# Optimization experiments

Measured on AMD Instinct MI355X. Metric: run time of the kernel, lower is better.

Reference implementation:

```python
import jax, jax.numpy as jnp
import numpy as np

NUM_EXPERTS = 8
HIDDEN = 2048
FFN = 1376
CAPACITY_FACTOR = 1.25
SCORE_SCALE = 1.0


def setup_inputs() -> dict:
    key = jax.random.key(0)
    k = jax.random.split(key, 6)
    T = 8192
    x = jax.random.normal(k[0], (T, HIDDEN), dtype=jnp.float32)
    topK_indices = jax.random.randint(k[1], (T,), 0, NUM_EXPERTS, dtype=jnp.int64)
    topK_scores = jax.random.uniform(k[2], (T,), dtype=jnp.float32)
    s = 1.0 / np.sqrt(HIDDEN)
    w_gate = jax.random.normal(k[3], (NUM_EXPERTS, HIDDEN, FFN), dtype=jnp.float32) * s
    w_up = jax.random.normal(k[4], (NUM_EXPERTS, HIDDEN, FFN), dtype=jnp.float32) * s
    w_down = jax.random.normal(k[5], (NUM_EXPERTS, FFN, HIDDEN), dtype=jnp.float32) * (1.0 / np.sqrt(FFN))
    return {"x": x, "topK_indices": topK_indices, "topK_scores": topK_scores,
            "w_gate": w_gate, "w_up": w_up, "w_down": w_down}


def reference(x, topK_indices, topK_scores, w_gate, w_up, w_down):
    T, D = x.shape
    E = w_gate.shape[0]
    capacity = int(CAPACITY_FACTOR * T / E)  # static (depends only on shapes)
    # position of each token within its assigned expert (deterministic drop:
    # keep the first `capacity` tokens in sequence order per expert)
    oh = jax.nn.one_hot(topK_indices, E, dtype=jnp.int32)          # [T,E]
    rank = jnp.take_along_axis(jnp.cumsum(oh, axis=0) - 1,
                               topK_indices[:, None].astype(jnp.int32), axis=1)[:, 0]
    keep = rank < capacity                                          # [T]
    # dispatch into per-expert capacity buffers; dropped tokens go to dummy slot
    slot = jnp.where(keep, topK_indices.astype(jnp.int32) * capacity + rank, E * capacity)
    buf = jnp.zeros((E * capacity + 1, D), x.dtype)
    buf = buf.at[slot].set(jnp.where(keep[:, None], x, jnp.zeros_like(x)))
    xe = buf[:E * capacity].reshape(E, capacity, D)                 # [E,C,D]
    # per-expert SwiGLU MLP as grouped GEMMs
    h = jax.nn.silu(jnp.einsum('ecd,edf->ecf', xe, w_gate)) * jnp.einsum('ecd,edf->ecf', xe, w_up)
    out = jnp.einsum('ecf,efd->ecd', h, w_down).reshape(E * capacity, D)
    out = jnp.concatenate([out, jnp.zeros((1, D), out.dtype)], axis=0)
    # combine: dropped tokens -> zero (dropped_padding='zero'), gate-score fusion
    y = out[slot] * keep[:, None].astype(out.dtype)
    y = y * (topK_scores[:, None] * SCORE_SCALE)
    return y
```

## Files before the change

### kernel.cpp

```cpp
#include <hip/hip_runtime.h>
#include <hip/hip_bf16.h>
#include <cstdint>
#include <cstddef>

#define NTOK 8192
#define DH   2048
#define DF   1376
#define NE   8
#define CAP  1280

typedef __bf16 bf16x8 __attribute__((ext_vector_type(8)));
typedef float  f32x4  __attribute__((ext_vector_type(4)));

#define BARRIER() asm volatile("s_barrier" ::: "memory")
#define WAITV(n)  asm volatile("s_waitcnt vmcnt(" #n ")" ::: "memory")
#define LGKM(n)   asm volatile("s_waitcnt lgkmcnt(" #n ")" ::: "memory")
#define SCHED0()  __builtin_amdgcn_sched_barrier(0)
#define SETPRIO(n) __builtin_amdgcn_s_setprio(n)

__device__ __forceinline__ uint32_t pk2(float a, float b) {
  float2 f; f.x = a; f.y = b;
  union { __hip_bfloat162 h; uint32_t u; } cv;
  cv.h = __float22bfloat162_rn(f);
  return cv.u;
}
__device__ __forceinline__ ushort bf16bits(float a) {
  return (ushort)(pk2(a, 0.f) & 0xFFFFu);
}
__device__ __forceinline__ void gload16(const ushort* g, ushort* l) {
  __builtin_amdgcn_global_load_lds(
      (const __attribute__((address_space(1))) uint32_t*)(const void*)g,
      (__attribute__((address_space(3))) uint32_t*)(void*)l,
      16, 0, 0);
}

__device__ __forceinline__ void rp_src(int o, int& row, int& ko) {
  int p = o >> 7;
  int g = ((o >> 4) & 7) ^ (p & 7);
  row = p * 2 + (g >> 2);
  ko  = (g & 3) * 8;
}
__device__ __forceinline__ int rp_off(int row, int l4) {
  return ((row >> 1) << 7) + (((((row & 1) << 2) + l4) ^ ((row >> 1) & 7)) << 4);
}

__global__ void routing_kernel(const int* __restrict__ idx, int* __restrict__ tok_slot,
                               int* __restrict__ tok_keep) {
  __shared__ int cnt[256][NE];
  const int t = threadIdx.x;
  for (int s = t; s < NE * CAP; s += 256) tok_slot[s] = -1;
  unsigned long long cA = 0ull, cB = 0ull;
  const int per = NTOK / 256, base = t * per;
  for (int i = 0; i < per; ++i) {
    int e = idx[base + i];
    unsigned long long inc = 1ull << ((e & 3) * 16);
    if (e < 4) cA += inc; else cB += inc;
  }
#pragma unroll
  for (int e = 0; e < 4; ++e) cnt[t][e]     = (int)((cA >> (e * 16)) & 0xFFFF);
#pragma unroll
  for (int e = 0; e < 4; ++e) cnt[t][4 + e] = (int)((cB >> (e * 16)) & 0xFFFF);
  __syncthreads();
  if (t < NE) {
    int run = 0;
    for (int i = 0; i < 256; ++i) { int c = cnt[i][t]; cnt[i][t] = run; run += c; }
  }
  __syncthreads();
  cA = 0ull; cB = 0ull;
#pragma unroll
  for (int e = 0; e < 4; ++e) cA |= (unsigned long long)(cnt[t][e] & 0xFFFF) << (e * 16);
#pragma unroll
  for (int e = 0; e < 4; ++e) cB |= (unsigned long long)(cnt[t][4 + e] & 0xFFFF) << (e * 16);
  for (int i = 0; i < per; ++i) {
    int token = base + i;
    int e = idx[token];
    int sh = (e & 3) * 16;
    int r = (int)(((e < 4 ? cA : cB) >> sh) & 0xFFFF);
    unsigned long long inc = 1ull << sh;
    if (e < 4) cA += inc; else cB += inc;
    bool keep = (r < CAP);
    tok_keep[token] = keep ? 1 : 0;
    if (keep) tok_slot[e * CAP + r] = token;
  }
}

__global__ __launch_bounds__(256) void prep_all(
    const float* __restrict__ wg, const float* __restrict__ wu, const float* __restrict__ wd,
    ushort* __restrict__ wgt, ushort* __restrict__ wut, ushort* __restrict__ wdt,
    const float* __restrict__ x, const int* __restrict__ keep,
    ushort* __restrict__ xb, float* __restrict__ y) {
  const int z = blockIdx.z;
  const int tid = threadIdx.x;
  if (z >= 24) {
    const int row = (z - 24) * 1024 + blockIdx.y * 32 + blockIdx.x;
    const int c = tid * 8;
    const size_t off = (size_t)row * DH + c;
    float4 a = *(const float4*)(x + off);
    float4 b = *(const float4*)(x + off + 4);
    uint4 p = { pk2(a.x, a.y), pk2(a.z, a.w), pk2(b.x, b.y), pk2(b.z, b.w) };
    *(uint4*)(xb + off) = p;
    if (!keep[row]) {
      float4 zz = {0.f, 0.f, 0.f, 0.f};
      *(float4*)(y + off) = zz;
      *(float4*)(y + off + 4) = zz;
    }
    return;
  }
  const float* in; ushort* out; int K, N, eidx;
  if (z < 8)       { in = wg; out = wgt; K = DH; N = DF; eidx = z; }
  else if (z < 16) { in = wu; out = wut; K = DH; N = DF; eidx = z - 8; }
  else             { in = wd; out = wdt; K = DF; N = DH; eidx = z - 16; }
  const int n0 = blockIdx.x * 64, k0 = blockIdx.y * 64;
  if (n0 >= N || k0 >= K) return;
  __shared__ ushort T[64][72];
  const size_t eoff_in  = (size_t)eidx * K * N;
  const size_t eoff_out = (size_t)eidx * N * K;
  const int kr = tid >> 4;
  const int nc = (tid & 15) * 4;
#pragma unroll
  for (int it = 0; it < 4; ++it) {
    int k = k0 + kr + it * 16;
    int n = n0 + nc;
    float4 v = {0.f, 0.f, 0.f, 0.f};
    if (k < K && n + 4 <= N) v = *(const float4*)(in + eoff_in + (size_t)k * N + n);
    T[nc + 0][kr + it * 16] = bf16bits(v.x);
    T[nc + 1][kr + it * 16] = bf16bits(v.y);
    T[nc + 2][kr + it * 16] = bf16bits(v.z);
    T[nc + 3][kr + it * 16] = bf16bits(v.w);
  }
  __syncthreads();
  const int nr = tid >> 2;
  const int kc = tid & 3;
#pragma unroll
  for (int it = 0; it < 2; ++it) {
    int kloc = kc * 16 + it * 8;
    int n = n0 + nr, k = k0 + kloc;
    if (n < N && k + 8 <= K)
      *(uint4*)(out + eoff_out + (size_t)n * K + k) = *(const uint4*)&T[nr][kloc];
  }
}

#define GU_READ(SET, RB) { \
  char* Ab_  = sm + (RB) * 16384; \
  char* Bgb_ = sm + 65536 + (RB) * 8192; \
  char* Bub_ = sm + 98304 + (RB) * 8192; \
  _Pragma("unroll") for (int i_ = 0; i_ < 4; ++i_) aR##SET[i_]  = *(const bf16x8*)(Ab_ + aoff[i_]); \
  _Pragma("unroll") for (int j_ = 0; j_ < 4; ++j_) bgR##SET[j_] = *(const bf16x8*)(Bgb_ + boff[j_]); \
  _Pragma("unroll") for (int j_ = 0; j_ < 4; ++j_) buR##SET[j_] = *(const bf16x8*)(Bub_ + boff[j_]); \
}
#define GU_MFMA(SET) { \
  _Pragma("unroll") for (int j_ = 0; j_ < 4; ++j_) \
    _Pragma("unroll") for (int i_ = 0; i_ < 4; ++i_) \
      accG[i_][j_] = __builtin_amdgcn_mfma_f32_16x16x32_bf16(aR##SET[i_], bgR##SET[j_], accG[i_][j_], 0, 0, 0); \
  _Pragma("unroll") for (int j_ = 0; j_ < 4; ++j_) \
    _Pragma("unroll") for (int i_ = 0; i_ < 4; ++i_) \
      accU[i_][j_] = __builtin_amdgcn_mfma_f32_16x16x32_bf16(aR##SET[i_], buR##SET[j_], accU[i_][j_], 0, 0, 0); \
}
#define GU_BODY(T, CUR, NXT) { \
  const int t_ = (T); \
  if (t_ + 3 < NT) { \
    const int kk_ = (t_ + 3) * 32; const int w_ = (t_ + 3) & 3; \
    gload16(srcA[0] + kk_, (ushort*)(sm + w_ * 16384 + dstw)); \
    gload16(srcA[1] + kk_, (ushort*)(sm + w_ * 16384 + 8192 + dstw)); \
    gload16(srcBg + kk_, (ushort*)(sm + 65536 + w_ * 8192 + dstw)); \
    gload16(srcBu + kk_, (ushort*)(sm + 98304 + w_ * 8192 + dstw)); \
  } \
  if (t_ + 1 < NT) { GU_READ(NXT, (t_ + 1) & 3); LGKM(12); } else { LGKM(0); } \
  SCHED0(); SETPRIO(1); \
  GU_MFMA(CUR); \
  SETPRIO(0); SCHED0(); \
  if (t_ + 3 < NT) { WAITV(4); } else if (t_ + 2 < NT) { WAITV(0); } \
  BARRIER(); \
}

__global__ __launch_bounds__(512, 2) void gemm_gateup3(
    const ushort* __restrict__ xb, const ushort* __restrict__ wgt,
    const ushort* __restrict__ wut, const int* __restrict__ tok_slot,
    ushort* __restrict__ h)
{
  __shared__ __align__(16) char sm[131072];
  const int tid = threadIdx.x, lane = tid & 63, wid = tid >> 6;
  const int wr = wid >> 1, wc = wid & 1;
  const int l15 = lane & 15, l4 = lane >> 4;

  int wgid = (blockIdx.x & 7) * 55 + (blockIdx.x >> 3);
  const int e = wgid / 55;
  const int rem = wgid - e * 55;
  const int mt = rem / 11, nt = rem - (rem / 11) * 11;
  const int n0 = nt * 128;

  const ushort* srcA[2]; const ushort* srcBg; const ushort* srcBu;
#pragma unroll
  for (int c = 0; c < 2; ++c) {
    int o = c * 8192 + wid * 1024 + lane * 16;
    int row, ko; rp_src(o, row, ko);
    int tk = tok_slot[e * CAP + mt * 256 + row];
    if (tk < 0) tk = 0;
    srcA[c] = xb + (size_t)tk * DH + ko;
  }
  {
    int o = wid * 1024 + lane * 16;
    int row, ko; rp_src(o, row, ko);
    int n = n0 + row; if (n > DF - 1) n = DF - 1;
    srcBg = wgt + ((size_t)e * DF + n) * DH + ko;
    srcBu = wut + ((size_t)e * DF + n) * DH + ko;
  }
  int aoff[4], boff[4];
#pragma unroll
  for (int i = 0; i < 4; ++i) aoff[i] = rp_off(wr * 64 + i * 16 + l15, l4);
#pragma unroll
  for (int j = 0; j < 4; ++j) boff[j] = rp_off(wc * 64 + j * 16 + l15, l4);
  const int dstw = wid * 1024;

  f32x4 accG[4][4], accU[4][4];
#pragma unroll
  for (int i = 0; i < 4; ++i)
#pragma unroll
    for (int j = 0; j < 4; ++j) {
      accG[i][j] = (f32x4){0.f, 0.f, 0.f, 0.f};
      accU[i][j] = (f32x4){0.f, 0.f, 0.f, 0.f};
    }

  const int NT = DH / 32;
#pragma unroll
  for (int t0 = 0; t0 < 3; ++t0) {
    int kk = t0 * 32;
    gload16(srcA[0] + kk, (ushort*)(sm + t0 * 16384 + dstw));
    gload16(srcA[1] + kk, (ushort*)(sm + t0 * 16384 + 8192 + dstw));
    gload16(srcBg   + kk, (ushort*)(sm + 65536 + t0 * 8192 + dstw));
    gload16(srcBu   + kk, (ushort*)(sm + 98304 + t0 * 8192 + dstw));
  }
  WAITV(4);
  BARRIER();

  bf16x8 aR0[4], bgR0[4], buR0[4], aR1[4], bgR1[4], buR1[4];
  GU_READ(0, 0);

  for (int t = 0; t < NT; t += 2) {
    GU_BODY(t, 0, 1);
    GU_BODY(t + 1, 1, 0);
  }

  const size_t rowbase = (size_t)(e * CAP + mt * 256 + wr * 64);
#pragma unroll
  for (int j = 0; j < 4; ++j) {
    int col = n0 + wc * 64 + j * 16 + l15;
    if (col < DF) {
#pragma unroll
      for (int i = 0; i < 4; ++i)
#pragma unroll
        for (int r2 = 0; r2 < 4; ++r2) {
          size_t row = rowbase + i * 16 + l4 * 4 + r2;
          float gv = accG[i][j][r2], uv = accU[i][j][r2];
          h[row * DF + col] = bf16bits(gv / (1.f + __expf(-gv)) * uv);
        }
    }
  }
}

#define DN_READ(SET, RB) { \
  char* Ab_ = sm + (RB) * 16384; \
  char* Bb_ = sm + 65536 + (RB) * 8192; \
  _Pragma("unroll") for (int i_ = 0; i_ < 4; ++i_) aR##SET[i_] = *(const bf16x8*)(Ab_ + aoff[i_]); \
  _Pragma("unroll") for (int j_ = 0; j_ < 4; ++j_) bR##SET[j_] = *(const bf16x8*)(Bb_ + boff[j_]); \
}
#define DN_MFMA(SET) { \
  _Pragma("unroll") for (int j_ = 0; j_ < 4; ++j_) \
    _Pragma("unroll") for (int i_ = 0; i_ < 4; ++i_) \
      acc[i_][j_] = __builtin_amdgcn_mfma_f32_16x16x32_bf16(aR##SET[i_], bR##SET[j_], acc[i_][j_], 0, 0, 0); \
}
#define DN_BODY(T, CUR, NXT) { \
  const int t_ = (T); \
  if (t_ + 3 < NT) { \
    const int kk_ = (t_ + 3) * 32; const int w_ = (t_ + 3) & 3; \
    gload16(srcA[0] + kk_, (ushort*)(sm + w_ * 16384 + dstw)); \
    gload16(srcA[1] + kk_, (ushort*)(sm + w_ * 16384 + 8192 + dstw)); \
    gload16(srcB + kk_, (ushort*)(sm + 65536 + w_ * 8192 + dstw)); \
  } \
  if (t_ + 1 < NT) { DN_READ(NXT, (t_ + 1) & 3); LGKM(8); } else { LGKM(0); } \
  SCHED0(); SETPRIO(1); \
  DN_MFMA(CUR); \
  SETPRIO(0); SCHED0(); \
  if (t_ + 3 < NT) { WAITV(3); } else if (t_ + 2 < NT) { WAITV(0); } \
  BARRIER(); \
}

__global__ __launch_bounds__(512, 2) void gemm_down3(
    const ushort* __restrict__ h, const ushort* __restrict__ wdt,
    const int* __restrict__ tok_slot, const float* __restrict__ scores,
    float* __restrict__ y)
{
  __shared__ __align__(16) char sm[100352];
  int* tokc = (int*)(sm + 98304);
  float* scc = (float*)(sm + 99328);
  const int tid = threadIdx.x, lane = tid & 63, wid = tid >> 6;
  const int wr = wid >> 1, wc = wid & 1;
  const int l15 = lane & 15, l4 = lane >> 4;

  int wgid = (blockIdx.x & 7) * 80 + (blockIdx.x >> 3);
  const int e = wgid / 80;
  const int rem = wgid - e * 80;
  const int mt = rem / 16, nt = rem & 15;
  const int n0 = nt * 128;

  if (tid < 256) {
    int tk = tok_slot[e * CAP + mt * 256 + tid];
    tokc[tid] = tk;
    scc[tid] = (tk >= 0) ? scores[tk] : 0.f;
  }
  __syncthreads();

  const size_t hrow0 = (size_t)(e * CAP + mt * 256);
  const ushort* srcA[2]; const ushort* srcB;
#pragma unroll
  for (int c = 0; c < 2; ++c) {
    int o = c * 8192 + wid * 1024 + lane * 16;
    int row, ko; rp_src(o, row, ko);
    srcA[c] = h + (hrow0 + row) * DF + ko;
  }
  {
    int o = wid * 1024 + lane * 16;
    int row, ko; rp_src(o, row, ko);
    srcB = wdt + ((size_t)e * DH + n0 + row) * DF + ko;
  }
  int aoff[4], boff[4];
#pragma unroll
  for (int i = 0; i < 4; ++i) aoff[i] = rp_off(wr * 64 + i * 16 + l15, l4);
#pragma unroll
  for (int j = 0; j < 4; ++j) boff[j] = rp_off(wc * 64 + j * 16 + l15, l4);
  const int dstw = wid * 1024;

  f32x4 acc[4][4];
#pragma unroll
  for (int i = 0; i < 4; ++i)
#pragma unroll
    for (int j = 0; j < 4; ++j) acc[i][j] = (f32x4){0.f, 0.f, 0.f, 0.f};

  const int NT = DF / 32;
#pragma unroll
  for (int t0 = 0; t0 < 3; ++t0) {
    int kk = t0 * 32;
    gload16(srcA[0] + kk, (ushort*)(sm + t0 * 16384 + dstw));
    gload16(srcA[1] + kk, (ushort*)(sm + t0 * 16384 + 8192 + dstw));
    gload16(srcB    + kk, (ushort*)(sm + 65536 + t0 * 8192 + dstw));
  }
  WAITV(3);
  BARRIER();

  bf16x8 aR0[4], bR0[4], aR1[4], bR1[4];
  DN_READ(0, 0);

  for (int t = 0; t < NT - 1; t += 2) {
    DN_BODY(t, 0, 1);
    DN_BODY(t + 1, 1, 0);
  }
  DN_BODY(NT - 1, 0, 1);

  int tkr[4][4]; float sr[4][4];
#pragma unroll
  for (int i = 0; i < 4; ++i)
#pragma unroll
    for (int r = 0; r < 4; ++r) {
      int rl = wr * 64 + i * 16 + l4 * 4 + r;
      tkr[i][r] = tokc[rl];
      sr[i][r]  = scc[rl];
    }
#pragma unroll
  for (int j = 0; j < 4; ++j) {
    int col = n0 + wc * 64 + j * 16 + l15;
#pragma unroll
    for (int i = 0; i < 4; ++i)
#pragma unroll
      for (int r = 0; r < 4; ++r)
        if (tkr[i][r] >= 0)
          y[(size_t)tkr[i][r] * DH + col] = acc[i][j][r] * sr[i][r];
  }
}

extern "C" void kernel_launch(void* const* d_in, const int* in_sizes, int n_in,
                              void* d_out, int out_size, void* d_ws, size_t ws_size,
                              hipStream_t stream) {
  const float* x   = (const float*)d_in[0];
  const int*   idx = (const int*)d_in[1];
  const float* sc  = (const float*)d_in[2];
  const float* wg  = (const float*)d_in[3];
  const float* wu  = (const float*)d_in[4];
  const float* wd  = (const float*)d_in[5];
  float* y = (float*)d_out;

  const size_t OFF_KEEP = 40960;
  const size_t OFF_H    = 73728;
  const size_t SZ_H     = (size_t)NE * CAP * DF * 2;
  const size_t OFF_XB   = OFF_H + SZ_H;
  const size_t SZ_XB    = (size_t)NTOK * DH * 2;
  const size_t OFF_WGT  = OFF_XB + SZ_XB;
  const size_t SZ_W     = (size_t)NE * DH * DF * 2;
  const size_t OFF_WUT  = OFF_WGT + SZ_W;
  const size_t OFF_WDT  = OFF_WUT + SZ_W;

  int* tok_slot = (int*)d_ws;
  int* tok_keep = (int*)((char*)d_ws + OFF_KEEP);
  ushort* hbuf = (ushort*)((char*)d_ws + OFF_H);
  ushort* xb   = (ushort*)((char*)d_ws + OFF_XB);
  ushort* wgt  = (ushort*)((char*)d_ws + OFF_WGT);
  ushort* wut  = (ushort*)((char*)d_ws + OFF_WUT);
  ushort* wdt  = (ushort*)((char*)d_ws + OFF_WDT);

  hipLaunchKernelGGL(routing_kernel, dim3(1), dim3(256), 0, stream, idx, tok_slot, tok_keep);
  hipLaunchKernelGGL(prep_all, dim3(32, 32, 32), dim3(256), 0, stream,
                     wg, wu, wd, wgt, wut, wdt, x, tok_keep, xb, y);
  hipLaunchKernelGGL(gemm_gateup3, dim3(440), dim3(512), 0, stream,
                     xb, wgt, wut, tok_slot, hbuf);
  hipLaunchKernelGGL(gemm_down3, dim3(640), dim3(512), 0, stream,
                     hbuf, wdt, tok_slot, sc, y);
}
```

Before: 321.6 us.

## Pre-tile activations and weights into swizzled K-tile-contiguous blocks for GEMMs

The prep kernels now write x, the gate/up weights, the down weights and the intermediate h directly into a blocked, pre-swizzled layout. Each 32-wide K tile of a 256- or 128-row block is contiguous there, so the GEMM kernels' global-to-LDS loads become linear strided copies with no token gather or per-row address computation. Token dispatch moves into the prep kernel through a token-to-slot map. The down-weight conversion becomes its own kernel launched after gate/up and reuses the gate weight buffer to shrink the workspace. Trade-offs are scattered writes during prep, an extra launch, and the loss of overlap for the down-weight conversion. Slots left unfilled for dropped tokens are never written, so they hold stale workspace data, but their outputs are discarded because tok_slot is -1.

```diff
diff --git a/kernel.cpp b/kernel.cpp
--- a/kernel.cpp
+++ b/kernel.cpp
@@ -34,18 +34,12 @@
       16, 0, 0);
 }
 
-__device__ __forceinline__ void rp_src(int o, int& row, int& ko) {
-  int p = o >> 7;
-  int g = ((o >> 4) & 7) ^ (p & 7);
-  row = p * 2 + (g >> 2);
-  ko  = (g & 3) * 8;
-}
 __device__ __forceinline__ int rp_off(int row, int l4) {
   return ((row >> 1) << 7) + (((((row & 1) << 2) + l4) ^ ((row >> 1) & 7)) << 4);
 }
 
 __global__ void routing_kernel(const int* __restrict__ idx, int* __restrict__ tok_slot,
-                               int* __restrict__ tok_keep) {
+                               int* __restrict__ tok2slot) {
   __shared__ int cnt[256][NE];
   const int t = threadIdx.x;
   for (int s = t; s < NE * CAP; s += 256) tok_slot[s] = -1;
@@ -79,42 +73,48 @@
     unsigned long long inc = 1ull << sh;
     if (e < 4) cA += inc; else cB += inc;
     bool keep = (r < CAP);
-    tok_keep[token] = keep ? 1 : 0;
+    tok2slot[token] = keep ? (e * CAP + r) : -1;
     if (keep) tok_slot[e * CAP + r] = token;
   }
 }
 
-__global__ __launch_bounds__(256) void prep_all(
-    const float* __restrict__ wg, const float* __restrict__ wu, const float* __restrict__ wd,
-    ushort* __restrict__ wgt, ushort* __restrict__ wut, ushort* __restrict__ wdt,
-    const float* __restrict__ x, const int* __restrict__ keep,
-    ushort* __restrict__ xb, float* __restrict__ y) {
+__global__ __launch_bounds__(256) void prep1(
+    const float* __restrict__ wg, const float* __restrict__ wu,
+    ushort* __restrict__ wgt, ushort* __restrict__ wut,
+    const float* __restrict__ x, const int* __restrict__ tok2slot,
+    ushort* __restrict__ xb2, float* __restrict__ y) {
   const int z = blockIdx.z;
   const int tid = threadIdx.x;
-  if (z >= 24) {
-    const int row = (z - 24) * 1024 + blockIdx.y * 32 + blockIdx.x;
-    const int c = tid * 8;
-    const size_t off = (size_t)row * DH + c;
+  if (z >= 16) {
+    const int row = (z - 16) * 1024 + blockIdx.y * 32 + blockIdx.x;
+    const int k0 = tid * 8;
+    const size_t off = (size_t)row * DH + k0;
     float4 a = *(const float4*)(x + off);
     float4 b = *(const float4*)(x + off + 4);
-    uint4 p = { pk2(a.x, a.y), pk2(a.z, a.w), pk2(b.x, b.y), pk2(b.z, b.w) };
-    *(uint4*)(xb + off) = p;
-    if (!keep[row]) {
+    uint4 p4 = { pk2(a.x, a.y), pk2(a.z, a.w), pk2(b.x, b.y), pk2(b.z, b.w) };
+    int slotg = tok2slot[row];
+    if (slotg < 0) {
       float4 zz = {0.f, 0.f, 0.f, 0.f};
       *(float4*)(y + off) = zz;
       *(float4*)(y + off + 4) = zz;
+    } else {
+      int e = slotg / CAP, srow = slotg - e * CAP;
+      int mt = srow >> 8, r = srow & 255;
+      int kt = k0 >> 5, kk = k0 & 31;
+      int p = r >> 1, g = ((r & 1) << 2) + (kk >> 3);
+      size_t ou = (size_t)((e * 5 + mt) * 64 + kt) * 8192 + p * 64 + ((g ^ (p & 7)) << 3);
+      *(uint4*)(xb2 + ou) = p4;
     }
     return;
   }
-  const float* in; ushort* out; int K, N, eidx;
-  if (z < 8)       { in = wg; out = wgt; K = DH; N = DF; eidx = z; }
-  else if (z < 16) { in = wu; out = wut; K = DH; N = DF; eidx = z - 8; }
-  else             { in = wd; out = wdt; K = DF; N = DH; eidx = z - 16; }
+  const float* in; ushort* out; int eidx;
+  if (z < 8) { in = wg; out = wgt; eidx = z; }
+  else       { in = wu; out = wut; eidx = z - 8; }
+  const int K = DH, N = DF;
   const int n0 = blockIdx.x * 64, k0 = blockIdx.y * 64;
-  if (n0 >= N || k0 >= K) return;
+  if (n0 >= N) return;
   __shared__ ushort T[64][72];
-  const size_t eoff_in  = (size_t)eidx * K * N;
-  const size_t eoff_out = (size_t)eidx * N * K;
+  const size_t eoff_in = (size_t)eidx * K * N;
   const int kr = tid >> 4;
   const int nc = (tid & 15) * 4;
 #pragma unroll
@@ -135,8 +135,51 @@
   for (int it = 0; it < 2; ++it) {
     int kloc = kc * 16 + it * 8;
     int n = n0 + nr, k = k0 + kloc;
-    if (n < N && k + 8 <= K)
-      *(uint4*)(out + eoff_out + (size_t)n * K + k) = *(const uint4*)&T[nr][kloc];
+    if (n < N && k + 8 <= K) {
+      int nt = n >> 7, r = n & 127;
+      int kt = k >> 5, kk = k & 31;
+      int p = r >> 1, g = ((r & 1) << 2) + (kk >> 3);
+      size_t ou = (size_t)((eidx * 11 + nt) * 64 + kt) * 4096 + p * 64 + ((g ^ (p & 7)) << 3);
+      *(uint4*)(out + ou) = *(const uint4*)&T[nr][kloc];
+    }
+  }
+}
+
+__global__ __launch_bounds__(256) void prep_wd(
+    const float* __restrict__ wd, ushort* __restrict__ wdt) {
+  const int eidx = blockIdx.z;
+  const int K = DF, N = DH;
+  const int n0 = blockIdx.x * 64, k0 = blockIdx.y * 64;
+  __shared__ ushort T[64][72];
+  const int tid = threadIdx.x;
+  const size_t eoff_in = (size_t)eidx * K * N;
+  const int kr = tid >> 4;
+  const int nc = (tid & 15) * 4;
+#pragma unroll
+  for (int it = 0; it < 4; ++it) {
+    int k = k0 + kr + it * 16;
+    int n = n0 + nc;
+    float4 v = {0.f, 0.f, 0.f, 0.f};
+    if (k < K && n + 4 <= N) v = *(const float4*)(wd + eoff_in + (size_t)k * N + n);
+    T[nc + 0][kr + it * 16] = bf16bits(v.x);
+    T[nc + 1][kr + it * 16] = bf16bits(v.y);
+    T[nc + 2][kr + it * 16] = bf16bits(v.z);
+    T[nc + 3][kr + it * 16] = bf16bits(v.w);
+  }
+  __syncthreads();
+  const int nr = tid >> 2;
+  const int kc = tid & 3;
+#pragma unroll
+  for (int it = 0; it < 2; ++it) {
+    int kloc = kc * 16 + it * 8;
+    int n = n0 + nr, k = k0 + kloc;
+    if (n < N && k + 8 <= K) {
+      int nt = n >> 7, r = n & 127;
+      int kt = k >> 5, kk = k & 31;
+      int p = r >> 1, g = ((r & 1) << 2) + (kk >> 3);
+      size_t ou = (size_t)((eidx * 16 + nt) * 43 + kt) * 4096 + p * 64 + ((g ^ (p & 7)) << 3);
+      *(uint4*)(wdt + ou) = *(const uint4*)&T[nr][kloc];
+    }
   }
 }
 
@@ -159,11 +202,11 @@
 #define GU_BODY(T, CUR, NXT) { \
   const int t_ = (T); \
   if (t_ + 3 < NT) { \
-    const int kk_ = (t_ + 3) * 32; const int w_ = (t_ + 3) & 3; \
-    gload16(srcA[0] + kk_, (ushort*)(sm + w_ * 16384 + dstw)); \
-    gload16(srcA[1] + kk_, (ushort*)(sm + w_ * 16384 + 8192 + dstw)); \
-    gload16(srcBg + kk_, (ushort*)(sm + 65536 + w_ * 8192 + dstw)); \
-    gload16(srcBu + kk_, (ushort*)(sm + 98304 + w_ * 8192 + dstw)); \
+    const int w_ = (t_ + 3) & 3; \
+    gload16(srcA[0] + (size_t)(t_ + 3) * 8192, (ushort*)(sm + w_ * 16384 + dstw)); \
+    gload16(srcA[1] + (size_t)(t_ + 3) * 8192, (ushort*)(sm + w_ * 16384 + 8192 + dstw)); \
+    gload16(srcBg + (size_t)(t_ + 3) * 4096, (ushort*)(sm + 65536 + w_ * 8192 + dstw)); \
+    gload16(srcBu + (size_t)(t_ + 3) * 4096, (ushort*)(sm + 98304 + w_ * 8192 + dstw)); \
   } \
   if (t_ + 1 < NT) { GU_READ(NXT, (t_ + 1) & 3); LGKM(12); } else { LGKM(0); } \
   SCHED0(); SETPRIO(1); \
@@ -174,9 +217,8 @@
 }
 
 __global__ __launch_bounds__(512, 2) void gemm_gateup3(
-    const ushort* __restrict__ xb, const ushort* __restrict__ wgt,
-    const ushort* __restrict__ wut, const int* __restrict__ tok_slot,
-    ushort* __restrict__ h)
+    const ushort* __restrict__ xb2, const ushort* __restrict__ wgt,
+    const ushort* __restrict__ wut, ushort* __restrict__ h)
 {
   __shared__ __align__(16) char sm[131072];
   const int tid = threadIdx.x, lane = tid & 63, wid = tid >> 6;
@@ -190,20 +232,14 @@
   const int n0 = nt * 128;
 
   const ushort* srcA[2]; const ushort* srcBg; const ushort* srcBu;
-#pragma unroll
-  for (int c = 0; c < 2; ++c) {
-    int o = c * 8192 + wid * 1024 + lane * 16;
-    int row, ko; rp_src(o, row, ko);
-    int tk = tok_slot[e * CAP + mt * 256 + row];
-    if (tk < 0) tk = 0;
-    srcA[c] = xb + (size_t)tk * DH + ko;
-  }
   {
-    int o = wid * 1024 + lane * 16;
-    int row, ko; rp_src(o, row, ko);
-    int n = n0 + row; if (n > DF - 1) n = DF - 1;
-    srcBg = wgt + ((size_t)e * DF + n) * DH + ko;
-    srcBu = wut + ((size_t)e * DF + n) * DH + ko;
+    const size_t abase = (size_t)((e * 5 + mt) * 64) * 8192;
+    const int lo = (wid * 1024 + lane * 16) >> 1;
+    srcA[0] = xb2 + abase + lo;
+    srcA[1] = xb2 + abase + 4096 + lo;
+    const size_t bbase = (size_t)((e * 11 + nt) * 64) * 4096;
+    srcBg = wgt + bbase + lo;
+    srcBu = wut + bbase + lo;
   }
   int aoff[4], boff[4];
 #pragma unroll
@@ -224,11 +260,10 @@
   const int NT = DH / 32;
 #pragma unroll
   for (int t0 = 0; t0 < 3; ++t0) {
-    int kk = t0 * 32;
-    gload16(srcA[0] + kk, (ushort*)(sm + t0 * 16384 + dstw));
-    gload16(srcA[1] + kk, (ushort*)(sm + t0 * 16384 + 8192 + dstw));
-    gload16(srcBg   + kk, (ushort*)(sm + 65536 + t0 * 8192 + dstw));
-    gload16(srcBu   + kk, (ushort*)(sm + 98304 + t0 * 8192 + dstw));
+    gload16(srcA[0] + (size_t)t0 * 8192, (ushort*)(sm + t0 * 16384 + dstw));
+    gload16(srcA[1] + (size_t)t0 * 8192, (ushort*)(sm + t0 * 16384 + 8192 + dstw));
+    gload16(srcBg + (size_t)t0 * 4096, (ushort*)(sm + 65536 + t0 * 8192 + dstw));
+    gload16(srcBu + (size_t)t0 * 4096, (ushort*)(sm + 98304 + t0 * 8192 + dstw));
   }
   WAITV(4);
   BARRIER();
@@ -241,18 +276,22 @@
     GU_BODY(t + 1, 1, 0);
   }
 
-  const size_t rowbase = (size_t)(e * CAP + mt * 256 + wr * 64);
+  const size_t hbase = (size_t)((e * 5 + mt) * 43) * 8192;
 #pragma unroll
   for (int j = 0; j < 4; ++j) {
     int col = n0 + wc * 64 + j * 16 + l15;
     if (col < DF) {
+      int kt = col >> 5, kk = col & 31;
+      int gb = kk >> 3, ke = kk & 7;
+      const size_t cb = hbase + (size_t)kt * 8192;
 #pragma unroll
       for (int i = 0; i < 4; ++i)
 #pragma unroll
         for (int r2 = 0; r2 < 4; ++r2) {
-          size_t row = rowbase + i * 16 + l4 * 4 + r2;
+          int rowloc = wr * 64 + i * 16 + l4 * 4 + r2;
+          int p = rowloc >> 1, g = ((rowloc & 1) << 2) + gb;
           float gv = accG[i][j][r2], uv = accU[i][j][r2];
-          h[row * DF + col] = bf16bits(gv / (1.f + __expf(-gv)) * uv);
+          h[cb + p * 64 + ((g ^ (p & 7)) << 3) + ke] = bf16bits(gv / (1.f + __expf(-gv)) * uv);
         }
     }
   }
@@ -272,10 +311,10 @@
 #define DN_BODY(T, CUR, NXT) { \
   const int t_ = (T); \
   if (t_ + 3 < NT) { \
-    const int kk_ = (t_ + 3) * 32; const int w_ = (t_ + 3) & 3; \
-    gload16(srcA[0] + kk_, (ushort*)(sm + w_ * 16384 + dstw)); \
-    gload16(srcA[1] + kk_, (ushort*)(sm + w_ * 16384 + 8192 + dstw)); \
-    gload16(srcB + kk_, (ushort*)(sm + 65536 + w_ * 8192 + dstw)); \
+    const int w_ = (t_ + 3) & 3; \
+    gload16(srcA[0] + (size_t)(t_ + 3) * 8192, (ushort*)(sm + w_ * 16384 + dstw)); \
+    gload16(srcA[1] + (size_t)(t_ + 3) * 8192, (ushort*)(sm + w_ * 16384 + 8192 + dstw)); \
+    gload16(srcB + (size_t)(t_ + 3) * 4096, (ushort*)(sm + 65536 + w_ * 8192 + dstw)); \
   } \
   if (t_ + 1 < NT) { DN_READ(NXT, (t_ + 1) & 3); LGKM(8); } else { LGKM(0); } \
   SCHED0(); SETPRIO(1); \
@@ -310,18 +349,13 @@
   }
   __syncthreads();
 
-  const size_t hrow0 = (size_t)(e * CAP + mt * 256);
   const ushort* srcA[2]; const ushort* srcB;
-#pragma unroll
-  for (int c = 0; c < 2; ++c) {
-    int o = c * 8192 + wid * 1024 + lane * 16;
-    int row, ko; rp_src(o, row, ko);
-    srcA[c] = h + (hrow0 + row) * DF + ko;
-  }
   {
-    int o = wid * 1024 + lane * 16;
-    int row, ko; rp_src(o, row, ko);
-    srcB = wdt + ((size_t)e * DH + n0 + row) * DF + ko;
+    const size_t abase = (size_t)((e * 5 + mt) * 43) * 8192;
+    const int lo = (wid * 1024 + lane * 16) >> 1;
+    srcA[0] = h + abase + lo;
+    srcA[1] = h + abase + 4096 + lo;
+    srcB = wdt + (size_t)((e * 16 + nt) * 43) * 4096 + lo;
   }
   int aoff[4], boff[4];
 #pragma unroll
@@ -339,10 +373,9 @@
   const int NT = DF / 32;
 #pragma unroll
   for (int t0 = 0; t0 < 3; ++t0) {
-    int kk = t0 * 32;
-    gload16(srcA[0] + kk, (ushort*)(sm + t0 * 16384 + dstw));
-    gload16(srcA[1] + kk, (ushort*)(sm + t0 * 16384 + 8192 + dstw));
-    gload16(srcB    + kk, (ushort*)(sm + 65536 + t0 * 8192 + dstw));
+    gload16(srcA[0] + (size_t)t0 * 8192, (ushort*)(sm + t0 * 16384 + dstw));
+    gload16(srcA[1] + (size_t)t0 * 8192, (ushort*)(sm + t0 * 16384 + 8192 + dstw));
+    gload16(srcB + (size_t)t0 * 4096, (ushort*)(sm + 65536 + t0 * 8192 + dstw));
   }
   WAITV(3);
   BARRIER();
@@ -388,29 +421,29 @@
   const float* wd  = (const float*)d_in[5];
   float* y = (float*)d_out;
 
-  const size_t OFF_KEEP = 40960;
-  const size_t OFF_H    = 73728;
-  const size_t SZ_H     = (size_t)NE * CAP * DF * 2;
-  const size_t OFF_XB   = OFF_H + SZ_H;
-  const size_t SZ_XB    = (size_t)NTOK * DH * 2;
-  const size_t OFF_WGT  = OFF_XB + SZ_XB;
-  const size_t SZ_W     = (size_t)NE * DH * DF * 2;
-  const size_t OFF_WUT  = OFF_WGT + SZ_W;
-  const size_t OFF_WDT  = OFF_WUT + SZ_W;
+  const size_t OFF_T2S = 40960;
+  const size_t OFF_H   = OFF_T2S + 32768;
+  const size_t SZ_H    = (size_t)NE * 5 * 43 * 16384;
+  const size_t OFF_XB  = OFF_H + SZ_H;
+  const size_t SZ_XB   = (size_t)NE * 5 * 64 * 16384;
+  const size_t OFF_WGT = OFF_XB + SZ_XB;
+  const size_t SZ_WG   = (size_t)NE * 11 * 64 * 8192;
+  const size_t OFF_WUT = OFF_WGT + SZ_WG;
 
   int* tok_slot = (int*)d_ws;
-  int* tok_keep = (int*)((char*)d_ws + OFF_KEEP);
+  int* tok2slot = (int*)((char*)d_ws + OFF_T2S);
   ushort* hbuf = (ushort*)((char*)d_ws + OFF_H);
-  ushort* xb   = (ushort*)((char*)d_ws + OFF_XB);
+  ushort* xb2  = (ushort*)((char*)d_ws + OFF_XB);
   ushort* wgt  = (ushort*)((char*)d_ws + OFF_WGT);
   ushort* wut  = (ushort*)((char*)d_ws + OFF_WUT);
-  ushort* wdt  = (ushort*)((char*)d_ws + OFF_WDT);
-
-  hipLaunchKernelGGL(routing_kernel, dim3(1), dim3(256), 0, stream, idx, tok_slot, tok_keep);
-  hipLaunchKernelGGL(prep_all, dim3(32, 32, 32), dim3(256), 0, stream,
-                     wg, wu, wd, wgt, wut, wdt, x, tok_keep, xb, y);
+  ushort* wdt  = wgt;
+
+  hipLaunchKernelGGL(routing_kernel, dim3(1), dim3(256), 0, stream, idx, tok_slot, tok2slot);
+  hipLaunchKernelGGL(prep1, dim3(32, 32, 24), dim3(256), 0, stream,
+                     wg, wu, wgt, wut, x, tok2slot, xb2, y);
   hipLaunchKernelGGL(gemm_gateup3, dim3(440), dim3(512), 0, stream,
-                     xb, wgt, wut, tok_slot, hbuf);
+                     xb2, wgt, wut, hbuf);
+  hipLaunchKernelGGL(prep_wd, dim3(32, 22, 8), dim3(256), 0, stream, wd, wdt);
   hipLaunchKernelGGL(gemm_down3, dim3(640), dim3(512), 0, stream,
                      hbuf, wdt, tok_slot, sc, y);
 }
```

Result: no change. 315.4 us, median of 2 (-1.9%).
